# Kernel optimization log

Measured on AMD Instinct MI355X. Metric: run time of the kernel, lower is better.

The kernel has to match this reference:

```python
import jax, jax.numpy as jnp
import numpy as np

SEQ_LEN = 8192
HIDDEN = 1024
NUM_SPANS = 4096
MAX_W = 32  # max span width (end - start + 1 <= MAX_W)
NEG_INF = -1e9


def setup_inputs() -> dict:
    key = jax.random.key(0)
    k_emb, k_s, k_w, k_aw = jax.random.split(key, 4)
    embeddings = jax.random.normal(k_emb, (1, SEQ_LEN, HIDDEN), dtype=jnp.float32)
    starts = jax.random.randint(k_s, (NUM_SPANS,), 0, SEQ_LEN - MAX_W, dtype=jnp.int32)
    widths = jax.random.randint(k_w, (NUM_SPANS,), 0, MAX_W, dtype=jnp.int32)  # width-1 in [0, MAX_W-1]
    ends = starts + widths
    attn_w = jax.random.normal(k_aw, (HIDDEN,), dtype=jnp.float32) * (HIDDEN ** -0.5)
    attn_b = jnp.zeros((), dtype=jnp.float32)
    return {"embeddings": embeddings, "starts": starts, "ends": ends,
            "attn_w": attn_w, "attn_b": attn_b}


def reference(embeddings, starts, ends, attn_w, attn_b):
    emb = embeddings[0]  # (S_len, H) -- original code indexes batch 0
    # Padded span positions: (num_spans, MAX_W)
    pos = starts[:, None] + jnp.arange(MAX_W, dtype=starts.dtype)[None, :]
    mask = pos <= ends[:, None]
    pos_c = jnp.minimum(pos, SEQ_LEN - 1)
    span_emb = emb[pos_c]  # (num_spans, MAX_W, H) gather
    # Linear(H -> 1) attention scores, masked softmax over span positions
    scores = jnp.einsum("swh,h->sw", span_emb, attn_w) + attn_b
    scores = jnp.where(mask, scores, NEG_INF)
    weights = jax.nn.softmax(scores, axis=1)
    attn_out = jnp.einsum("sw,swh->sh", weights, span_emb)
    start_emb = emb[starts]  # (num_spans, H)
    end_emb = emb[ends]
    return jnp.concatenate([start_emb, end_emb, attn_out], axis=-1)  # (num_spans, 3H)
```

## Files before the change

kernel.cpp:

```cpp
#include <hip/hip_runtime.h>
#include <math.h>

#define SEQ_LEN   8192
#define HIDDEN    1024
#define NUM_SPANS 4096
#define MAX_W     32

typedef float f4v __attribute__((ext_vector_type(4)));

__device__ __forceinline__ float dot4(float4 a, float4 b) {
    return a.x * b.x + a.y * b.y + a.z * b.z + a.w * b.w;
}

__device__ __forceinline__ void nt_store4(float4* p, float4 v) {
    f4v x = { v.x, v.y, v.z, v.w };
    __builtin_nontemporal_store(x, (f4v*)p);
}

__global__ __launch_bounds__(256, 4) void span_repr_kernel(
    const float* __restrict__ emb,
    const int* __restrict__ starts,
    const int* __restrict__ ends,
    const float* __restrict__ attn_w,
    const float* __restrict__ attn_b,
    float* __restrict__ out)
{
    const int tid = threadIdx.x;
    const int w2  = tid >> 6;
    const int c   = tid & 63;
    const int s   = (blockIdx.x << 2) + w2;

    const int start = starts[s];
    const int wmax  = ends[s] - start;
    const float bias = attn_b[0];

    const float4* __restrict__ embr = (const float4*)emb + (size_t)start * 256;

    const float4* __restrict__ wv4 = (const float4*)attn_w;
    const float4 wv0 = wv4[c];
    const float4 wv1 = wv4[c + 64];
    const float4 wv2 = wv4[c + 128];
    const float4 wv3 = wv4[c + 192];

    float4* __restrict__ out4 = (float4*)(out + (size_t)s * (3 * HIDDEN));

    float4 v0 = embr[c];
    float4 v1 = embr[c + 64];
    float4 v2 = embr[c + 128];
    float4 v3 = embr[c + 192];

    nt_store4(&out4[c],       v0);
    nt_store4(&out4[c + 64],  v1);
    nt_store4(&out4[c + 128], v2);
    nt_store4(&out4[c + 192], v3);

    float4 a0 = make_float4(0.f, 0.f, 0.f, 0.f);
    float4 a1 = make_float4(0.f, 0.f, 0.f, 0.f);
    float4 a2 = make_float4(0.f, 0.f, 0.f, 0.f);
    float4 a3 = make_float4(0.f, 0.f, 0.f, 0.f);
    float m = -INFINITY;
    float l = 0.0f;

    for (int r = 0; r <= wmax; ++r) {
        const float4* __restrict__ nr = embr + (size_t)min(r + 1, wmax) * 256;
        float4 n0 = nr[c];
        float4 n1 = nr[c + 64];
        float4 n2 = nr[c + 128];
        float4 n3 = nr[c + 192];
        __builtin_amdgcn_sched_barrier(0);

        float p = dot4(v0, wv0) + dot4(v1, wv1) + dot4(v2, wv2) + dot4(v3, wv3);
        #pragma unroll
        for (int off = 32; off > 0; off >>= 1)
            p += __shfl_xor(p, off, 64);
        const float sc = p + bias;

        if (sc > m) {
            const float alpha = __expf(m - sc);
            a0.x *= alpha; a0.y *= alpha; a0.z *= alpha; a0.w *= alpha;
            a1.x *= alpha; a1.y *= alpha; a1.z *= alpha; a1.w *= alpha;
            a2.x *= alpha; a2.y *= alpha; a2.z *= alpha; a2.w *= alpha;
            a3.x *= alpha; a3.y *= alpha; a3.z *= alpha; a3.w *= alpha;
            l *= alpha;
            m = sc;
        }
        const float e = __expf(sc - m);
        l += e;
        a0.x += e * v0.x; a0.y += e * v0.y; a0.z += e * v0.z; a0.w += e * v0.w;
        a1.x += e * v1.x; a1.y += e * v1.y; a1.z += e * v1.z; a1.w += e * v1.w;
        a2.x += e * v2.x; a2.y += e * v2.y; a2.z += e * v2.z; a2.w += e * v2.w;
        a3.x += e * v3.x; a3.y += e * v3.y; a3.z += e * v3.z; a3.w += e * v3.w;

        v0 = n0; v1 = n1; v2 = n2; v3 = n3;
    }

    nt_store4(&out4[256 + c],       v0);
    nt_store4(&out4[256 + c + 64],  v1);
    nt_store4(&out4[256 + c + 128], v2);
    nt_store4(&out4[256 + c + 192], v3);

    const float inv = 1.0f / l;
    nt_store4(&out4[512 + c],
              make_float4(a0.x * inv, a0.y * inv, a0.z * inv, a0.w * inv));
    nt_store4(&out4[512 + c + 64],
              make_float4(a1.x * inv, a1.y * inv, a1.z * inv, a1.w * inv));
    nt_store4(&out4[512 + c + 128],
              make_float4(a2.x * inv, a2.y * inv, a2.z * inv, a2.w * inv));
    nt_store4(&out4[512 + c + 192],
              make_float4(a3.x * inv, a3.y * inv, a3.z * inv, a3.w * inv));
}

extern "C" void kernel_launch(void* const* d_in, const int* in_sizes, int n_in,
                              void* d_out, int out_size, void* d_ws, size_t ws_size,
                              hipStream_t stream) {
    const float* emb    = (const float*)d_in[0];
    const int*   starts = (const int*)d_in[1];
    const int*   ends   = (const int*)d_in[2];
    const float* attn_w = (const float*)d_in[3];
    const float* attn_b = (const float*)d_in[4];
    float* out = (float*)d_out;

    span_repr_kernel<<<NUM_SPANS / 4, 256, 0, stream>>>(emb, starts, ends, attn_w, attn_b, out);
}
```

Before: 124.2 us.

## Sort spans by start and remap blocks per XCD for cache locality

Adds a single-block counting-sort kernel that buckets spans by start position (bins of 8 rows) and writes a permutation to workspace. The main kernel reads spans in that order and remaps block IDs so that each XCD handles a contiguous range of sorted spans. Overlapping spans then share embedding rows within one XCD's L2, which should cut HBM re-reads. The cost is an extra serial kernel launch plus a dependent indirection load before each span's work starts.

```diff
diff --git a/kernel.cpp b/kernel.cpp
--- a/kernel.cpp
+++ b/kernel.cpp
@@ -5,6 +5,8 @@
 #define HIDDEN    1024
 #define NUM_SPANS 4096
 #define MAX_W     32
+#define NBLK      (NUM_SPANS / 4)
+#define NXCD      8
 
 typedef float f4v __attribute__((ext_vector_type(4)));
 
@@ -17,18 +19,75 @@
     __builtin_nontemporal_store(x, (f4v*)p);
 }
 
+__global__ __launch_bounds__(1024) void sort_spans_kernel(
+    const int* __restrict__ starts,
+    int* __restrict__ perm)
+{
+    __shared__ int hist[1024];
+    __shared__ int base[1024];
+    __shared__ int wsum[16];
+
+    const int tid  = threadIdx.x;
+    const int lane = tid & 63;
+    const int wid  = tid >> 6;
+
+    hist[tid] = 0;
+    __syncthreads();
+
+    #pragma unroll
+    for (int i = tid; i < NUM_SPANS; i += 1024)
+        atomicAdd(&hist[starts[i] >> 3], 1);
+    __syncthreads();
+
+    const int v = hist[tid];
+    int sc = v;
+    #pragma unroll
+    for (int off = 1; off < 64; off <<= 1) {
+        const int t = __shfl_up(sc, off, 64);
+        if (lane >= off) sc += t;
+    }
+    if (lane == 63) wsum[wid] = sc;
+    __syncthreads();
+    if (wid == 0 && lane < 16) {
+        int ws = wsum[lane];
+        #pragma unroll
+        for (int off = 1; off < 16; off <<= 1) {
+            const int t = __shfl_up(ws, off, 64);
+            if (lane >= off) ws += t;
+        }
+        wsum[lane] = ws;
+    }
+    __syncthreads();
+    const int waveOff = (wid == 0) ? 0 : wsum[wid - 1];
+    base[tid] = waveOff + sc - v;
+    __syncthreads();
+
+    hist[tid] = 0;
+    __syncthreads();
+
+    #pragma unroll
+    for (int i = tid; i < NUM_SPANS; i += 1024) {
+        const int b   = starts[i] >> 3;
+        const int pos = base[b] + atomicAdd(&hist[b], 1);
+        perm[pos] = i;
+    }
+}
+
 __global__ __launch_bounds__(256, 4) void span_repr_kernel(
     const float* __restrict__ emb,
     const int* __restrict__ starts,
     const int* __restrict__ ends,
     const float* __restrict__ attn_w,
     const float* __restrict__ attn_b,
+    const int* __restrict__ perm,
     float* __restrict__ out)
 {
     const int tid = threadIdx.x;
     const int w2  = tid >> 6;
     const int c   = tid & 63;
-    const int s   = (blockIdx.x << 2) + w2;
+
+    const int slot = (blockIdx.x & (NXCD - 1)) * (NBLK / NXCD) + (blockIdx.x >> 3);
+    const int s    = perm[(slot << 2) + w2];
 
     const int start = starts[s];
     const int wmax  = ends[s] - start;
@@ -120,5 +179,8 @@
     const float* attn_b = (const float*)d_in[4];
     float* out = (float*)d_out;
 
-    span_repr_kernel<<<NUM_SPANS / 4, 256, 0, stream>>>(emb, starts, ends, attn_w, attn_b, out);
+    int* perm = (int*)d_ws;
+
+    sort_spans_kernel<<<1, 1024, 0, stream>>>(starts, perm);
+    span_repr_kernel<<<NBLK, 256, 0, stream>>>(emb, starts, ends, attn_w, attn_b, perm, out);
 }
```

New measurement: 113.0 us. 1.1x faster.
